# Kernel tuning notes

Measured on AMD Instinct MI355X. Metric: run time of the kernel, lower is better.

## Reference

```python
import jax, jax.numpy as jnp
import numpy as np

DIM = 128
EDGE_FEAT_DIM = 2
N_NODES = 50000
N_EDGES = 600000
EPS = 1e-5


def setup_inputs() -> dict:
    key = jax.random.key(0)
    ks = jax.random.split(key, 16)
    d = DIM
    inp = {}
    inp["x"] = jax.random.normal(ks[0], (N_NODES, d), dtype=jnp.float32)
    inp["edge_index"] = jax.random.randint(ks[1], (2, N_EDGES), 0, N_NODES, dtype=jnp.int32)
    inp["edge_weight_norm"] = jax.random.uniform(ks[2], (N_EDGES,), dtype=jnp.float32)
    inp["edge_feat"] = jax.random.normal(ks[3], (N_EDGES, EDGE_FEAT_DIM), dtype=jnp.float32)
    inp["batch"] = jnp.zeros((N_NODES,), dtype=jnp.int32)
    # phi: Linear(dim, dim)
    inp["W_phi"] = jax.random.normal(ks[4], (d, d), dtype=jnp.float32) * (1.0 / np.sqrt(d))
    inp["b_phi"] = jnp.zeros((d,), dtype=jnp.float32)
    # edge_gate: Linear(2d+2, d) -> BN(d) -> GELU -> Linear(d, 1)
    din = 2 * d + EDGE_FEAT_DIM
    inp["W_g1"] = jax.random.normal(ks[5], (din, d), dtype=jnp.float32) * (1.0 / np.sqrt(din))
    inp["b_g1"] = jnp.zeros((d,), dtype=jnp.float32)
    inp["bn_gamma"] = jnp.ones((d,), dtype=jnp.float32)
    inp["bn_beta"] = jnp.zeros((d,), dtype=jnp.float32)
    inp["bn_mean"] = jnp.zeros((d,), dtype=jnp.float32)
    inp["bn_var"] = jnp.ones((d,), dtype=jnp.float32)
    inp["W_g2"] = jax.random.normal(ks[6], (d, 1), dtype=jnp.float32) * (1.0 / np.sqrt(d))
    inp["b_g2"] = jnp.zeros((1,), dtype=jnp.float32)
    # upd: Linear(2d, d)
    inp["W_u"] = jax.random.normal(ks[7], (2 * d, d), dtype=jnp.float32) * (1.0 / np.sqrt(2 * d))
    inp["b_u"] = jnp.zeros((d,), dtype=jnp.float32)
    # LayerNorm(dim)
    inp["ln_gamma"] = jnp.ones((d,), dtype=jnp.float32)
    inp["ln_beta"] = jnp.zeros((d,), dtype=jnp.float32)
    return inp


def reference(x, edge_index, edge_weight_norm, edge_feat, batch,
              W_phi, b_phi, W_g1, b_g1, bn_gamma, bn_beta, bn_mean, bn_var,
              W_g2, b_g2, W_u, b_u, ln_gamma, ln_beta):
    src, dst = edge_index[0], edge_index[1]
    # phi(x): [N, d]
    xj = x @ W_phi + b_phi
    # edge gate MLP on [x_dst, x_src, e]: [E, 2d+2]
    g_in = jnp.concatenate([x[dst], x[src], edge_feat], axis=-1)
    h1 = g_in @ W_g1 + b_g1
    h1 = (h1 - bn_mean) * jax.lax.rsqrt(bn_var + EPS) * bn_gamma + bn_beta  # BN eval mode
    h1 = jax.nn.gelu(h1, approximate=False)
    gate = jax.nn.sigmoid(h1 @ W_g2 + b_g2)[:, 0]  # [E]
    # messages and scatter-add aggregation
    msg = xj[src] * (edge_weight_norm * gate)[:, None]  # [E, d]
    agg = jax.ops.segment_sum(msg, dst, num_segments=x.shape[0])  # [N, d]
    # update MLP + GELU + residual + LayerNorm
    h = jnp.concatenate([x, agg], axis=-1) @ W_u + b_u
    h = jax.nn.gelu(h, approximate=False)
    y = x + h
    mu = jnp.mean(y, axis=-1, keepdims=True)
    var = jnp.var(y, axis=-1, keepdims=True)
    return (y - mu) * jax.lax.rsqrt(var + EPS) * ln_gamma + ln_beta
```

## Files before the change

kernel.cpp:

```cpp
#include <hip/hip_runtime.h>
#include <hip/hip_fp16.h>
#include <math.h>

#define DIM 128
#define NN 50000
#define NE 600000
#define EPS 1e-5f
#define CAP 64

struct H8 { __half2 h[4]; };
struct F8 { float4 a, b; };

typedef _Float16 f16x8 __attribute__((ext_vector_type(8)));
typedef float    f32x4 __attribute__((ext_vector_type(4)));

__device__ __forceinline__ float gelu_fast(float x) {
    const float c1 = 2.3022085f;
    const float c2 = 0.1029437f;
    const float x2 = x * x;
    const float z  = x * __builtin_fmaf(c2, x2, c1);
    const float u  = __builtin_amdgcn_exp2f(z);
    const float r  = __builtin_amdgcn_rcpf(1.f + u);
    return __builtin_fmaf(-x, r, x);
}

__device__ __forceinline__ float sigmoid_fast(float y) {
    const float u = __builtin_amdgcn_exp2f(-1.4426950409f * y);
    return __builtin_amdgcn_rcpf(1.f + u);
}

__global__ __launch_bounds__(256) void k_prep_scale(
    const float* __restrict__ Wg1, const float* __restrict__ bg1,
    const float* __restrict__ bng, const float* __restrict__ bnb,
    const float* __restrict__ bnm, const float* __restrict__ bnv,
    __half* __restrict__ WABth, float* __restrict__ bA,
    float* __restrict__ w0p, float* __restrict__ w1p)
{
    const int k = blockIdx.x;
    const int t = threadIdx.x;
    const int c = t & 127;
    const float s = bng[c] * rsqrtf(bnv[c] + EPS);
    const float w = (t < 128) ? Wg1[k * DIM + c] : Wg1[(DIM + k) * DIM + c];
    WABth[t * DIM + k] = __float2half(w * s);
    if (k == 0 && t < 128) {
        const float tt = bnb[c] - bnm[c] * s;
        bA[c]  = bg1[c] * s + tt;
        w0p[c] = Wg1[256 * DIM + c] * s;
        w1p[c] = Wg1[257 * DIM + c] * s;
    }
}

__global__ __launch_bounds__(128) void k_prep_wpu(
    const float* __restrict__ Wphi, const float* __restrict__ bphi,
    const float* __restrict__ Wu,
    __half* __restrict__ Wct, float* __restrict__ bpu)
{
    const int a = blockIdx.x;
    const int j = threadIdx.x;
    float acc = 0.f;
    #pragma unroll 8
    for (int k = 0; k < DIM; ++k)
        acc += Wphi[a * DIM + k] * Wu[(DIM + k) * DIM + j];
    Wct[j * 256 + a]       = __float2half(Wu[a * DIM + j]);
    Wct[j * 256 + 128 + a] = __float2half(acc);
    if (a == 0) {
        float b = 0.f;
        #pragma unroll 8
        for (int k = 0; k < DIM; ++k)
            b += bphi[k] * Wu[(DIM + k) * DIM + j];
        bpu[j] = b;
    }
}

__global__ __launch_bounds__(256) void k_node_mfma(
    const float* __restrict__ x, const __half* __restrict__ WABth,
    const float* __restrict__ bA,
    __half* __restrict__ A, __half* __restrict__ Bv, __half* __restrict__ xh)
{
    __shared__ __half xs[64][136];
    __shared__ __half ys[64][136];

    const int t    = threadIdx.x;
    const int wv   = t >> 6;
    const int lane = t & 63;
    const int n16  = lane & 15;
    const int quad = lane >> 4;
    const int m0   = blockIdx.x * 64;

    #pragma unroll
    for (int i = 0; i < 4; ++i) {
        const int idx = i * 256 + t;
        const int row = idx >> 4;
        const int col = (idx & 15) * 8;
        const int grow = min(m0 + row, NN - 1);
        const float4 xa = *(const float4*)(x + (size_t)grow * DIM + col);
        const float4 xb = *(const float4*)(x + (size_t)grow * DIM + col + 4);
        f16x8 af;
        af[0] = (_Float16)xa.x; af[1] = (_Float16)xa.y;
        af[2] = (_Float16)xa.z; af[3] = (_Float16)xa.w;
        af[4] = (_Float16)xb.x; af[5] = (_Float16)xb.y;
        af[6] = (_Float16)xb.z; af[7] = (_Float16)xb.w;
        *(f16x8*)&xs[row][col] = af;
        *(f16x8*)(xh + (size_t)grow * DIM + col) = af;
    }
    __syncthreads();

    f32x4 acc[4][4];
    #pragma unroll
    for (int mt = 0; mt < 4; ++mt)
        #pragma unroll
        for (int nt = 0; nt < 4; ++nt)
            acc[mt][nt] = (f32x4){0.f, 0.f, 0.f, 0.f};

    #pragma unroll
    for (int ks = 0; ks < 4; ++ks) {
        const int ko = ks * 32 + quad * 8;
        f16x8 bf[4];
        #pragma unroll
        for (int nt = 0; nt < 4; ++nt) {
            const int c = wv * 64 + nt * 16 + n16;
            bf[nt] = *(const f16x8*)(WABth + c * DIM + ko);
        }
        #pragma unroll
        for (int mt = 0; mt < 4; ++mt) {
            const f16x8 af = *(const f16x8*)&xs[mt * 16 + n16][ko];
            #pragma unroll
            for (int nt = 0; nt < 4; ++nt)
                acc[mt][nt] = __builtin_amdgcn_mfma_f32_16x16x32_f16(
                    af, bf[nt], acc[mt][nt], 0, 0, 0);
        }
    }
    __syncthreads();

    #pragma unroll
    for (int nt = 0; nt < 4; ++nt) {
        const int c = wv * 64 + nt * 16 + n16;
        const float bias = (c < 128) ? bA[c] : 0.f;
        #pragma unroll
        for (int mt = 0; mt < 4; ++mt)
            #pragma unroll
            for (int reg = 0; reg < 4; ++reg) {
                const int row = mt * 16 + quad * 4 + reg;
                const __half hv = __float2half(acc[mt][nt][reg] + bias);
                if (c < 128) xs[row][c]       = hv;
                else         ys[row][c - 128] = hv;
            }
    }
    __syncthreads();

    #pragma unroll
    for (int i = 0; i < 8; ++i) {
        const int chunk = t + i * 256;
        const int row = chunk >> 5;
        const int o   = (chunk & 31) * 8;
        if (m0 + row < NN) {
            if (o < 128) {
                const uint4 v = *(const uint4*)&xs[row][o];
                *(uint4*)(A + (size_t)(m0 + row) * DIM + o) = v;
            } else {
                const uint4 v = *(const uint4*)&ys[row][o - 128];
                *(uint4*)(Bv + (size_t)(m0 + row) * DIM + o - 128) = v;
            }
        }
    }
}

__global__ __launch_bounds__(256) void k_gate(
    const int*   __restrict__ ei,  const float* __restrict__ ew,
    const float* __restrict__ ef,
    const __half* __restrict__ A,  const __half* __restrict__ Bv,
    const float* __restrict__ w0p, const float* __restrict__ w1p,
    const float* __restrict__ Wg2, const float* __restrict__ bg2,
    int* __restrict__ deg, int2* __restrict__ pairs)
{
    const int t    = threadIdx.x;
    const int lane = t & 63;
    const int sub  = lane >> 4;
    const int sl   = lane & 15;
    const int c8   = sl * 8;
    const int e0   = (blockIdx.x * 4 + (t >> 6)) * 8 + sub * 2;

    const F8 WG = *(const F8*)(Wg2 + c8);
    const F8 W0 = *(const F8*)(w0p + c8);
    const F8 W1 = *(const F8*)(w1p + c8);
    const float bg2v = bg2[0];
    const float* w0 = (const float*)&W0;
    const float* w1 = (const float*)&W1;
    const float* wg = (const float*)&WG;

    const int2   srcs = *(const int2*)(ei + e0);
    const int2   dsts = *(const int2*)(ei + NE + e0);
    const float4 efv  = *(const float4*)(ef + 2 * e0);
    const float2 ewv  = *(const float2*)(ew + e0);

    const H8 a0 = *(const H8*)(A  + (size_t)dsts.x * DIM + c8);
    const H8 b0 = *(const H8*)(Bv + (size_t)srcs.x * DIM + c8);
    const H8 a1 = *(const H8*)(A  + (size_t)dsts.y * DIM + c8);
    const H8 b1 = *(const H8*)(Bv + (size_t)srcs.y * DIM + c8);

    float p0 = 0.f, p1 = 0.f;
    #pragma unroll
    for (int i = 0; i < 4; ++i) {
        const float2 s0 = __half22float2(__hadd2(a0.h[i], b0.h[i]));
        const float2 s1 = __half22float2(__hadd2(a1.h[i], b1.h[i]));
        const int c0 = 2 * i, c1 = 2 * i + 1;
        float h;
        h = s0.x + efv.x * w0[c0] + efv.y * w1[c0];
        p0 = __builtin_fmaf(gelu_fast(h), wg[c0], p0);
        h = s0.y + efv.x * w0[c1] + efv.y * w1[c1];
        p0 = __builtin_fmaf(gelu_fast(h), wg[c1], p0);
        h = s1.x + efv.z * w0[c0] + efv.w * w1[c0];
        p1 = __builtin_fmaf(gelu_fast(h), wg[c0], p1);
        h = s1.y + efv.z * w0[c1] + efv.w * w1[c1];
        p1 = __builtin_fmaf(gelu_fast(h), wg[c1], p1);
    }
    #pragma unroll
    for (int off = 1; off < 16; off <<= 1) {
        p0 += __shfl_xor(p0, off, 64);
        p1 += __shfl_xor(p1, off, 64);
    }

    if (sl == 0) {
        const float coef0 = ewv.x * sigmoid_fast(p0 + bg2v);
        const float coef1 = ewv.y * sigmoid_fast(p1 + bg2v);
        const int pos0 = atomicAdd(&deg[dsts.x], 1);
        if (pos0 < CAP)
            pairs[(size_t)dsts.x * CAP + pos0] = make_int2(srcs.x, __float_as_int(coef0));
        const int pos1 = atomicAdd(&deg[dsts.y], 1);
        if (pos1 < CAP)
            pairs[(size_t)dsts.y * CAP + pos1] = make_int2(srcs.y, __float_as_int(coef1));
    }
}

__global__ __launch_bounds__(128, 3) void k_agg_update(
    const int* __restrict__ deg, const int2* __restrict__ pairs,
    const __half* __restrict__ xh, const __half* __restrict__ Wct,
    const float* __restrict__ bu, const float* __restrict__ bpu,
    const float* __restrict__ lng, const float* __restrict__ lnb,
    float* __restrict__ out)
{
    __shared__ __half xt[16][136];
    __shared__ __half at[2][16][136];
    __shared__ float  sct[2][16];
    __shared__ float  sred_s[2][16];
    __shared__ float  sred_ss[2][16];

    const int t    = threadIdx.x;
    const int w    = t >> 6;
    const int lane = t & 63;
    const int n16  = lane & 15;
    const int quad = lane >> 4;
    const int m0   = blockIdx.x * 16;

    const int slot = quad;
    const int sl   = n16;
    const int c8   = sl * 8;

    int    cnt[4];
    size_t pb[4];
    #pragma unroll
    for (int r = 0; r < 4; ++r) {
        const int lr = r * 4 + slot;
        const int nc = min(m0 + lr, NN - 1);
        const int d  = min(deg[nc], CAP);
        const int h  = ((d + 2) >> 2) << 1;
        const int lo = w ? h : 0;
        const int hi = w ? d : h;
        cnt[r] = hi - lo;
        pb[r]  = (size_t)nc * CAP + lo;
    }

    #pragma unroll
    for (int i = 0; i < 2; ++i) {
        const int idx = i * 128 + t;
        const int row = idx >> 4;
        const int col = (idx & 15) * 8;
        const int grow = min(m0 + row, NN - 1);
        *(f16x8*)&xt[row][col] = *(const f16x8*)(xh + (size_t)grow * DIM + col);
    }

    float acc[4][8];
    float scn[4] = {0.f, 0.f, 0.f, 0.f};
    #pragma unroll
    for (int r = 0; r < 4; ++r)
        #pragma unroll
        for (int i = 0; i < 8; ++i) acc[r][i] = 0.f;

    const int cmax = max(max(cnt[0], cnt[1]), max(cnt[2], cnt[3]));

    for (int jj = 0; jj < cmax; jj += 4) {
        int4 pq0[4], pq1[4];
        #pragma unroll
        for (int r = 0; r < 4; ++r) {
            pq0[r] = *(const int4*)(&pairs[pb[r] + jj]);
            pq1[r] = *(const int4*)(&pairs[pb[r] + jj + 2]);
        }

        int   ix[16];
        float cf[16];
        #pragma unroll
        for (int r = 0; r < 4; ++r) {
            const int q = 4 * r;
            const bool v0 = (jj     < cnt[r]);
            const bool v1 = (jj + 1 < cnt[r]);
            const bool v2 = (jj + 2 < cnt[r]);
            const bool v3 = (jj + 3 < cnt[r]);
            ix[q]     = v0 ? pq0[r].x : 0;
            cf[q]     = v0 ? __int_as_float(pq0[r].y) : 0.f;
            ix[q + 1] = v1 ? pq0[r].z : 0;
            cf[q + 1] = v1 ? __int_as_float(pq0[r].w) : 0.f;
            ix[q + 2] = v2 ? pq1[r].x : 0;
            cf[q + 2] = v2 ? __int_as_float(pq1[r].y) : 0.f;
            ix[q + 3] = v3 ? pq1[r].z : 0;
            cf[q + 3] = v3 ? __int_as_float(pq1[r].w) : 0.f;
        }

        H8 xv[16];
        #pragma unroll
        for (int q = 0; q < 16; ++q)
            xv[q] = *(const H8*)(xh + (size_t)ix[q] * DIM + c8);

        #pragma unroll
        for (int r = 0; r < 4; ++r) {
            #pragma unroll
            for (int k = 0; k < 4; ++k) {
                const int   q = 4 * r + k;
                const float c = cf[q];
                #pragma unroll
                for (int i = 0; i < 4; ++i) {
                    const float2 f = __half22float2(xv[q].h[i]);
                    acc[r][2 * i]     = __builtin_fmaf(c, f.x, acc[r][2 * i]);
                    acc[r][2 * i + 1] = __builtin_fmaf(c, f.y, acc[r][2 * i + 1]);
                }
                scn[r] += c;
            }
        }
    }

    #pragma unroll
    for (int r = 0; r < 4; ++r) {
        const int lr = r * 4 + slot;
        f16x8 hv;
        #pragma unroll
        for (int i = 0; i < 8; ++i) hv[i] = (_Float16)acc[r][i];
        *(f16x8*)&at[w][lr][c8] = hv;
        if (sl == 0) sct[w][lr] = scn[r];
    }
    __syncthreads();

    f32x4 acc2[4];
    #pragma unroll
    for (int nt = 0; nt < 4; ++nt) acc2[nt] = (f32x4){0.f, 0.f, 0.f, 0.f};

    const int rloc = n16;
    #pragma unroll
    for (int ks = 0; ks < 4; ++ks) {
        const int ko = ks * 32 + quad * 8;
        const f16x8 af = *(const f16x8*)&xt[rloc][ko];
        #pragma unroll
        for (int nt = 0; nt < 4; ++nt) {
            const int c = w * 64 + nt * 16 + n16;
            const f16x8 bf = *(const f16x8*)(Wct + c * 256 + ko);
            acc2[nt] = __builtin_amdgcn_mfma_f32_16x16x32_f16(af, bf, acc2[nt], 0, 0, 0);
        }
    }
    #pragma unroll
    for (int half = 0; half < 2; ++half) {
        #pragma unroll
        for (int ks = 0; ks < 4; ++ks) {
            const int ko = ks * 32 + quad * 8;
            const f16x8 af = *(const f16x8*)&at[half][rloc][ko];
            #pragma unroll
            for (int nt = 0; nt < 4; ++nt) {
                const int c = w * 64 + nt * 16 + n16;
                const f16x8 bf = *(const f16x8*)(Wct + c * 256 + 128 + ko);
                acc2[nt] = __builtin_amdgcn_mfma_f32_16x16x32_f16(af, bf, acc2[nt], 0, 0, 0);
            }
        }
    }

    int   rl[4];
    float scv[4];
    #pragma unroll
    for (int reg = 0; reg < 4; ++reg) {
        rl[reg]  = quad * 4 + reg;
        scv[reg] = sct[0][rl[reg]] + sct[1][rl[reg]];
    }

    float yv[4][4];
    float s[4]  = {0.f, 0.f, 0.f, 0.f};
    float ss[4] = {0.f, 0.f, 0.f, 0.f};

    #pragma unroll
    for (int nt = 0; nt < 4; ++nt) {
        const int c = w * 64 + nt * 16 + n16;
        const float buv = bu[c], bpv = bpu[c];
        #pragma unroll
        for (int reg = 0; reg < 4; ++reg) {
            float h = acc2[nt][reg] + buv + scv[reg] * bpv;
            h = gelu_fast(h);
            const float xv = __half2float(xt[rl[reg]][c]);
            const float y = xv + h;
            yv[nt][reg] = y;
            s[reg]  += y;
            ss[reg] += y * y;
        }
    }

    #pragma unroll
    for (int reg = 0; reg < 4; ++reg) {
        #pragma unroll
        for (int off = 1; off < 16; off <<= 1) {
            s[reg]  += __shfl_xor(s[reg],  off, 64);
            ss[reg] += __shfl_xor(ss[reg], off, 64);
        }
    }
    if (n16 == 0) {
        #pragma unroll
        for (int reg = 0; reg < 4; ++reg) {
            sred_s[w][rl[reg]]  = s[reg];
            sred_ss[w][rl[reg]] = ss[reg];
        }
    }
    __syncthreads();

    float mu[4], rs[4];
    #pragma unroll
    for (int reg = 0; reg < 4; ++reg) {
        const float stot  = sred_s[0][rl[reg]]  + sred_s[1][rl[reg]];
        const float sstot = sred_ss[0][rl[reg]] + sred_ss[1][rl[reg]];
        mu[reg] = stot * (1.f / DIM);
        const float var = sstot * (1.f / DIM) - mu[reg] * mu[reg];
        rs[reg] = rsqrtf(var + EPS);
    }

    #pragma unroll
    for (int nt = 0; nt < 4; ++nt) {
        const int c = w * 64 + nt * 16 + n16;
        const float gg = lng[c], bb2 = lnb[c];
        #pragma unroll
        for (int reg = 0; reg < 4; ++reg) {
            const int grow = m0 + rl[reg];
            if (grow < NN)
                __builtin_nontemporal_store(
                    (yv[nt][reg] - mu[reg]) * rs[reg] * gg + bb2,
                    &out[(size_t)grow * DIM + c]);
        }
    }
}

extern "C" void kernel_launch(void* const* d_in, const int* in_sizes, int n_in,
                              void* d_out, int out_size, void* d_ws, size_t ws_size,
                              hipStream_t stream)
{
    const float* x    = (const float*)d_in[0];
    const int*   ei   = (const int*)  d_in[1];
    const float* ew   = (const float*)d_in[2];
    const float* ef   = (const float*)d_in[3];
    const float* Wphi = (const float*)d_in[5];
    const float* bphi = (const float*)d_in[6];
    const float* Wg1  = (const float*)d_in[7];
    const float* bg1  = (const float*)d_in[8];
    const float* bng  = (const float*)d_in[9];
    const float* bnb  = (const float*)d_in[10];
    const float* bnm  = (const float*)d_in[11];
    const float* bnv  = (const float*)d_in[12];
    const float* Wg2  = (const float*)d_in[13];
    const float* bg2  = (const float*)d_in[14];
    const float* Wu   = (const float*)d_in[15];
    const float* bu   = (const float*)d_in[16];
    const float* lng  = (const float*)d_in[17];
    const float* lnb  = (const float*)d_in[18];

    float* out = (float*)d_out;

    char* wsb = (char*)d_ws;
    size_t off = 0;
    auto carve = [&](size_t bytes) -> void* {
        void* p = wsb + off;
        off += (bytes + 255) & ~(size_t)255;
        return p;
    };
    __half* xh    = (__half*)carve((size_t)NN * DIM * 2);
    __half* A     = (__half*)carve((size_t)NN * DIM * 2);
    __half* Bv    = (__half*)carve((size_t)NN * DIM * 2);
    __half* WABth = (__half*)carve(256 * DIM * 2);
    __half* Wct   = (__half*)carve(DIM * 256 * 2);
    float*  bA    = (float*) carve(DIM * 4);
    float*  w0p   = (float*) carve(DIM * 4);
    float*  w1p   = (float*) carve(DIM * 4);
    float*  bpu   = (float*) carve(DIM * 4);
    int*    deg   = (int*)   carve((size_t)NN * 4);
    int2*   pairs = (int2*)  carve((size_t)NN * CAP * 8 + 256);

    hipMemsetAsync(deg, 0, (size_t)NN * 4, stream);

    k_prep_scale<<<128, 256, 0, stream>>>(Wg1, bg1, bng, bnb, bnm, bnv,
                                          WABth, bA, w0p, w1p);
    k_prep_wpu<<<128, 128, 0, stream>>>(Wphi, bphi, Wu, Wct, bpu);
    k_node_mfma<<<(NN + 63) / 64, 256, 0, stream>>>(x, WABth, bA, A, Bv, xh);
    k_gate<<<NE / 32, 256, 0, stream>>>(ei, ew, ef, A, Bv, w0p, w1p, Wg2, bg2,
                                        deg, pairs);
    k_agg_update<<<(NN + 15) / 16, 128, 0, stream>>>(deg, pairs, xh, Wct,
                                                     bu, bpu, lng, lnb, out);
}
```

Baseline: 252.6 us.

## Merge prep kernels and widen node and aggregation kernels to more waves

New measurement: 258.5 us. 2.3% more time.

```diff
diff --git a/kernel.cpp b/kernel.cpp
--- a/kernel.cpp
+++ b/kernel.cpp
@@ -29,50 +29,51 @@
     return __builtin_amdgcn_rcpf(1.f + u);
 }
 
-__global__ __launch_bounds__(256) void k_prep_scale(
+__global__ __launch_bounds__(256) void k_prep(
     const float* __restrict__ Wg1, const float* __restrict__ bg1,
     const float* __restrict__ bng, const float* __restrict__ bnb,
     const float* __restrict__ bnm, const float* __restrict__ bnv,
-    __half* __restrict__ WABth, float* __restrict__ bA,
-    float* __restrict__ w0p, float* __restrict__ w1p)
-{
-    const int k = blockIdx.x;
-    const int t = threadIdx.x;
-    const int c = t & 127;
-    const float s = bng[c] * rsqrtf(bnv[c] + EPS);
-    const float w = (t < 128) ? Wg1[k * DIM + c] : Wg1[(DIM + k) * DIM + c];
-    WABth[t * DIM + k] = __float2half(w * s);
-    if (k == 0 && t < 128) {
-        const float tt = bnb[c] - bnm[c] * s;
-        bA[c]  = bg1[c] * s + tt;
-        w0p[c] = Wg1[256 * DIM + c] * s;
-        w1p[c] = Wg1[257 * DIM + c] * s;
-    }
-}
-
-__global__ __launch_bounds__(128) void k_prep_wpu(
     const float* __restrict__ Wphi, const float* __restrict__ bphi,
     const float* __restrict__ Wu,
+    __half* __restrict__ WABth, float* __restrict__ bA,
+    float* __restrict__ w0p, float* __restrict__ w1p,
     __half* __restrict__ Wct, float* __restrict__ bpu)
 {
-    const int a = blockIdx.x;
-    const int j = threadIdx.x;
-    float acc = 0.f;
-    #pragma unroll 8
-    for (int k = 0; k < DIM; ++k)
-        acc += Wphi[a * DIM + k] * Wu[(DIM + k) * DIM + j];
-    Wct[j * 256 + a]       = __float2half(Wu[a * DIM + j]);
-    Wct[j * 256 + 128 + a] = __float2half(acc);
-    if (a == 0) {
-        float b = 0.f;
-        #pragma unroll 8
-        for (int k = 0; k < DIM; ++k)
-            b += bphi[k] * Wu[(DIM + k) * DIM + j];
-        bpu[j] = b;
-    }
-}
-
-__global__ __launch_bounds__(256) void k_node_mfma(
+    if (blockIdx.x < 128) {
+        const int k = blockIdx.x;
+        const int t = threadIdx.x;
+        const int c = t & 127;
+        const float s = bng[c] * rsqrtf(bnv[c] + EPS);
+        const float w = (t < 128) ? Wg1[k * DIM + c] : Wg1[(DIM + k) * DIM + c];
+        WABth[t * DIM + k] = __float2half(w * s);
+        if (k == 0 && t < 128) {
+            const float tt = bnb[c] - bnm[c] * s;
+            bA[c]  = bg1[c] * s + tt;
+            w0p[c] = Wg1[256 * DIM + c] * s;
+            w1p[c] = Wg1[257 * DIM + c] * s;
+        }
+    } else {
+        const int a = blockIdx.x - 128;
+        const int j = threadIdx.x;
+        if (j < 128) {
+            float acc = 0.f;
+            #pragma unroll 8
+            for (int k = 0; k < DIM; ++k)
+                acc += Wphi[a * DIM + k] * Wu[(DIM + k) * DIM + j];
+            Wct[j * 256 + a]       = __float2half(Wu[a * DIM + j]);
+            Wct[j * 256 + 128 + a] = __float2half(acc);
+            if (a == 0) {
+                float b = 0.f;
+                #pragma unroll 8
+                for (int k = 0; k < DIM; ++k)
+                    b += bphi[k] * Wu[(DIM + k) * DIM + j];
+                bpu[j] = b;
+            }
+        }
+    }
+}
+
+__global__ __launch_bounds__(512) void k_node_mfma(
     const float* __restrict__ x, const __half* __restrict__ WABth,
     const float* __restrict__ bA,
     __half* __restrict__ A, __half* __restrict__ Bv, __half* __restrict__ xh)
@@ -88,8 +89,8 @@
     const int m0   = blockIdx.x * 64;
 
     #pragma unroll
-    for (int i = 0; i < 4; ++i) {
-        const int idx = i * 256 + t;
+    for (int i = 0; i < 2; ++i) {
+        const int idx = i * 512 + t;
         const int row = idx >> 4;
         const int col = (idx & 15) * 8;
         const int grow = min(m0 + row, NN - 1);
@@ -105,27 +106,27 @@
     }
     __syncthreads();
 
-    f32x4 acc[4][4];
+    f32x4 acc[4][2];
     #pragma unroll
     for (int mt = 0; mt < 4; ++mt)
         #pragma unroll
-        for (int nt = 0; nt < 4; ++nt)
+        for (int nt = 0; nt < 2; ++nt)
             acc[mt][nt] = (f32x4){0.f, 0.f, 0.f, 0.f};
 
     #pragma unroll
     for (int ks = 0; ks < 4; ++ks) {
         const int ko = ks * 32 + quad * 8;
-        f16x8 bf[4];
-        #pragma unroll
-        for (int nt = 0; nt < 4; ++nt) {
-            const int c = wv * 64 + nt * 16 + n16;
+        f16x8 bf[2];
+        #pragma unroll
+        for (int nt = 0; nt < 2; ++nt) {
+            const int c = wv * 32 + nt * 16 + n16;
             bf[nt] = *(const f16x8*)(WABth + c * DIM + ko);
         }
         #pragma unroll
         for (int mt = 0; mt < 4; ++mt) {
             const f16x8 af = *(const f16x8*)&xs[mt * 16 + n16][ko];
             #pragma unroll
-            for (int nt = 0; nt < 4; ++nt)
+            for (int nt = 0; nt < 2; ++nt)
                 acc[mt][nt] = __builtin_amdgcn_mfma_f32_16x16x32_f16(
                     af, bf[nt], acc[mt][nt], 0, 0, 0);
         }
@@ -133,8 +134,8 @@
     __syncthreads();
 
     #pragma unroll
-    for (int nt = 0; nt < 4; ++nt) {
-        const int c = wv * 64 + nt * 16 + n16;
+    for (int nt = 0; nt < 2; ++nt) {
+        const int c = wv * 32 + nt * 16 + n16;
         const float bias = (c < 128) ? bA[c] : 0.f;
         #pragma unroll
         for (int mt = 0; mt < 4; ++mt)
@@ -149,8 +150,8 @@
     __syncthreads();
 
     #pragma unroll
-    for (int i = 0; i < 8; ++i) {
-        const int chunk = t + i * 256;
+    for (int i = 0; i < 4; ++i) {
+        const int chunk = t + i * 512;
         const int row = chunk >> 5;
         const int o   = (chunk & 31) * 8;
         if (m0 + row < NN) {
@@ -232,7 +233,7 @@
     }
 }
 
-__global__ __launch_bounds__(128, 3) void k_agg_update(
+__global__ __launch_bounds__(256, 3) void k_agg_update(
     const int* __restrict__ deg, const int2* __restrict__ pairs,
     const __half* __restrict__ xh, const __half* __restrict__ Wct,
     const float* __restrict__ bu, const float* __restrict__ bpu,
@@ -240,10 +241,10 @@
     float* __restrict__ out)
 {
     __shared__ __half xt[16][136];
-    __shared__ __half at[2][16][136];
-    __shared__ float  sct[2][16];
-    __shared__ float  sred_s[2][16];
-    __shared__ float  sred_ss[2][16];
+    __shared__ __half at[4][16][136];
+    __shared__ float  sct[4][16];
+    __shared__ float  sred_s[4][16];
+    __shared__ float  sred_ss[4][16];
 
     const int t    = threadIdx.x;
     const int w    = t >> 6;
@@ -263,18 +264,15 @@
         const int lr = r * 4 + slot;
         const int nc = min(m0 + lr, NN - 1);
         const int d  = min(deg[nc], CAP);
-        const int h  = ((d + 2) >> 2) << 1;
-        const int lo = w ? h : 0;
-        const int hi = w ? d : h;
+        const int lo = (((w * d) >> 2) + 1) & ~1;
+        const int hi = (w < 3) ? (((((w + 1) * d) >> 2) + 1) & ~1) : d;
         cnt[r] = hi - lo;
         pb[r]  = (size_t)nc * CAP + lo;
     }
 
-    #pragma unroll
-    for (int i = 0; i < 2; ++i) {
-        const int idx = i * 128 + t;
-        const int row = idx >> 4;
-        const int col = (idx & 15) * 8;
+    {
+        const int row = t >> 4;
+        const int col = (t & 15) * 8;
         const int grow = min(m0 + row, NN - 1);
         *(f16x8*)&xt[row][col] = *(const f16x8*)(xh + (size_t)grow * DIM + col);
     }
@@ -348,9 +346,9 @@
     }
     __syncthreads();
 
-    f32x4 acc2[4];
-    #pragma unroll
-    for (int nt = 0; nt < 4; ++nt) acc2[nt] = (f32x4){0.f, 0.f, 0.f, 0.f};
+    f32x4 acc2[2];
+    #pragma unroll
+    for (int nt = 0; nt < 2; ++nt) acc2[nt] = (f32x4){0.f, 0.f, 0.f, 0.f};
 
     const int rloc = n16;
     #pragma unroll
@@ -358,21 +356,21 @@
         const int ko = ks * 32 + quad * 8;
         const f16x8 af = *(const f16x8*)&xt[rloc][ko];
         #pragma unroll
-        for (int nt = 0; nt < 4; ++nt) {
-            const int c = w * 64 + nt * 16 + n16;
+        for (int nt = 0; nt < 2; ++nt) {
+            const int c = w * 32 + nt * 16 + n16;
             const f16x8 bf = *(const f16x8*)(Wct + c * 256 + ko);
             acc2[nt] = __builtin_amdgcn_mfma_f32_16x16x32_f16(af, bf, acc2[nt], 0, 0, 0);
         }
     }
     #pragma unroll
-    for (int half = 0; half < 2; ++half) {
+    for (int half = 0; half < 4; ++half) {
         #pragma unroll
         for (int ks = 0; ks < 4; ++ks) {
             const int ko = ks * 32 + quad * 8;
             const f16x8 af = *(const f16x8*)&at[half][rloc][ko];
             #pragma unroll
-            for (int nt = 0; nt < 4; ++nt) {
-                const int c = w * 64 + nt * 16 + n16;
+            for (int nt = 0; nt < 2; ++nt) {
+                const int c = w * 32 + nt * 16 + n16;
                 const f16x8 bf = *(const f16x8*)(Wct + c * 256 + 128 + ko);
                 acc2[nt] = __builtin_amdgcn_mfma_f32_16x16x32_f16(af, bf, acc2[nt], 0, 0, 0);
             }
@@ -384,16 +382,17 @@
     #pragma unroll
     for (int reg = 0; reg < 4; ++reg) {
         rl[reg]  = quad * 4 + reg;
-        scv[reg] = sct[0][rl[reg]] + sct[1][rl[reg]];
-    }
-
-    float yv[4][4];
+        scv[reg] = sct[0][rl[reg]] + sct[1][rl[reg]]
+                 + sct[2][rl[reg]] + sct[3][rl[reg]];
+    }
+
+    float yv[2][4];
     float s[4]  = {0.f, 0.f, 0.f, 0.f};
     float ss[4] = {0.f, 0.f, 0.f, 0.f};
 
     #pragma unroll
-    for (int nt = 0; nt < 4; ++nt) {
-        const int c = w * 64 + nt * 16 + n16;
+    for (int nt = 0; nt < 2; ++nt) {
+        const int c = w * 32 + nt * 16 + n16;
         const float buv = bu[c], bpv = bpu[c];
         #pragma unroll
         for (int reg = 0; reg < 4; ++reg) {
@@ -427,16 +426,18 @@
     float mu[4], rs[4];
     #pragma unroll
     for (int reg = 0; reg < 4; ++reg) {
-        const float stot  = sred_s[0][rl[reg]]  + sred_s[1][rl[reg]];
-        const float sstot = sred_ss[0][rl[reg]] + sred_ss[1][rl[reg]];
+        const float stot  = sred_s[0][rl[reg]]  + sred_s[1][rl[reg]]
+                          + sred_s[2][rl[reg]]  + sred_s[3][rl[reg]];
+        const float sstot = sred_ss[0][rl[reg]] + sred_ss[1][rl[reg]]
+                          + sred_ss[2][rl[reg]] + sred_ss[3][rl[reg]];
         mu[reg] = stot * (1.f / DIM);
         const float var = sstot * (1.f / DIM) - mu[reg] * mu[reg];
         rs[reg] = rsqrtf(var + EPS);
     }
 
     #pragma unroll
-    for (int nt = 0; nt < 4; ++nt) {
-        const int c = w * 64 + nt * 16 + n16;
+    for (int nt = 0; nt < 2; ++nt) {
+        const int c = w * 32 + nt * 16 + n16;
         const float gg = lng[c], bb2 = lnb[c];
         #pragma unroll
         for (int reg = 0; reg < 4; ++reg) {
@@ -495,12 +496,12 @@
 
     hipMemsetAsync(deg, 0, (size_t)NN * 4, stream);
 
-    k_prep_scale<<<128, 256, 0, stream>>>(Wg1, bg1, bng, bnb, bnm, bnv,
-                                          WABth, bA, w0p, w1p);
-    k_prep_wpu<<<128, 128, 0, stream>>>(Wphi, bphi, Wu, Wct, bpu);
-    k_node_mfma<<<(NN + 63) / 64, 256, 0, stream>>>(x, WABth, bA, A, Bv, xh);
+    k_prep<<<256, 256, 0, stream>>>(Wg1, bg1, bng, bnb, bnm, bnv,
+                                    Wphi, bphi, Wu,
+                                    WABth, bA, w0p, w1p, Wct, bpu);
+    k_node_mfma<<<(NN + 63) / 64, 512, 0, stream>>>(x, WABth, bA, A, Bv, xh);
     k_gate<<<NE / 32, 256, 0, stream>>>(ei, ew, ef, A, Bv, w0p, w1p, Wg2, bg2,
                                         deg, pairs);
-    k_agg_update<<<(NN + 15) / 16, 128, 0, stream>>>(deg, pairs, xh, Wct,
+    k_agg_update<<<(NN + 15) / 16, 256, 0, stream>>>(deg, pairs, xh, Wct,
                                                      bu, bpu, lng, lnb, out);
 }
```
